# Performance work log

Hardware: AMD Instinct MI355X
Metric: run time of the kernel (lower is better)

Reference implementation:

```python
import jax, jax.numpy as jnp
import numpy as np


def setup_inputs() -> dict:
    key = jax.random.key(0)
    ks = jax.random.split(key, 6)
    B, H, W, C = 2, 96, 96, 64
    x = jax.random.normal(ks[0], (B, H, W, C), dtype=jnp.float32)
    # 1x1 conv weights as [C_in, C_out] matrices (kernel size 1)
    W1 = jax.random.normal(ks[1], (C, C // 8), dtype=jnp.float32) * 0.1
    b1 = jnp.zeros((C // 8,), dtype=jnp.float32)
    W2 = jax.random.normal(ks[2], (C, C // 8), dtype=jnp.float32) * 0.1
    b2 = jnp.zeros((C // 8,), dtype=jnp.float32)
    W3 = jax.random.normal(ks[3], (C, C // 2), dtype=jnp.float32) * 0.1
    b3 = jnp.zeros((C // 2,), dtype=jnp.float32)
    W4 = jax.random.normal(ks[4], (C // 2, C), dtype=jnp.float32) * 0.1
    b4 = jnp.zeros((C,), dtype=jnp.float32)
    gamma = jax.random.uniform(ks[5], (1,), dtype=jnp.float32)
    return {"x": x, "W1": W1, "b1": b1, "W2": W2, "b2": b2,
            "W3": W3, "b3": b3, "W4": W4, "b4": b4, "gamma": gamma}


def reference(x, W1, b1, W2, b2, W3, b3, W4, b4, gamma):
    B, H, W_, C = x.shape
    N = H * W_
    # 1x1 convs == per-pixel matmuls
    f = jnp.einsum('bhwc,cd->bhwd', x, W1) + b1   # [B,H,W,C/8] (key)
    g = jnp.einsum('bhwc,cd->bhwd', x, W2) + b2   # [B,H,W,C/8] (query)
    h = jnp.einsum('bhwc,cd->bhwd', x, W3) + b3   # [B,H,W,C/2] (value)
    f = f.reshape(B, N, -1)
    g = g.reshape(B, N, -1)
    h = h.reshape(B, N, -1)
    s = jnp.einsum('bnd,bmd->bnm', g, f)          # [B,N,N] full score matrix
    beta = jax.nn.softmax(s, axis=-1)
    o = jnp.einsum('bnm,bmd->bnd', beta, h)       # [B,N,C/2]
    o = o.reshape(B, H, W_, C // 2)
    o = jnp.einsum('bhwc,cd->bhwd', o, W4) + b4   # [B,H,W,C]
    return gamma[0] * o + x
```

## Files before the change

### kernel.cpp

```cpp
#include <hip/hip_runtime.h>
#include <hip/hip_bf16.h>


#define BATCH 2
#define NTOK 9216
#define CCH 64
#define DV 32
#define KS 8
#define KEYS_PER_BLOCK (NTOK / KS)
#define KEYS_PER_WAVE (KEYS_PER_BLOCK / 2)
#define KT 32
#define NKT (KEYS_PER_WAVE / KT)
#define ROWS (BATCH * NTOK)
#define QTB (ROWS / 64)
#define NKTILE (NTOK / 32)
#define LOG2E 1.44269504088896340736f
#define PB 32
#define ZTOT 152064

typedef __attribute__((ext_vector_type(8))) short bf16x8;
typedef __attribute__((ext_vector_type(4))) float f32x4;

__device__ __forceinline__ short f2bf(float x) {
    __hip_bfloat16 h = __float2bfloat16(x);
    return *(short*)&h;
}
__device__ __forceinline__ float bf2f(short s) {
    unsigned u = ((unsigned)(unsigned short)s) << 16;
    return *(float*)&u;
}

__global__ __launch_bounds__(512) void proj_kernel(
    const float* __restrict__ x,
    const float* __restrict__ W1, const float* __restrict__ b1,
    const float* __restrict__ W2, const float* __restrict__ b2,
    const float* __restrict__ W3, const float* __restrict__ b3,
    short* __restrict__ fx, short* __restrict__ gx, short* __restrict__ hTi,
    float4* __restrict__ zbase)
{
    __shared__ float xS[PB][CCH];
    __shared__ short fgS[2][PB][32];
    __shared__ short hS[32][PB + 2];

    const int tid = threadIdx.x;
    const int r0  = blockIdx.x * PB;

    {
        int zi = blockIdx.x * 512 + tid;
        if (zi < ZTOT) zbase[zi] = make_float4(0.f, 0.f, 0.f, 0.f);
    }

    ((float4*)xS)[tid] = ((const float4*)(x + (size_t)r0 * CCH))[tid];
    __syncthreads();

    {
        const int half = tid >> 8;
        const int rr   = (tid & 255) >> 3;
        const int c    = tid & 7;
        const float* xr = xS[rr];
        if (half == 0) {
            float acc = b1[c];
            #pragma unroll
            for (int k = 0; k < CCH; ++k) acc += xr[k] * W1[k * 8 + c];
            short hi = f2bf(acc);
            short lo = f2bf(acc - bf2f(hi));
            fgS[0][rr][c] = hi; fgS[0][rr][c + 8] = hi;
            fgS[0][rr][c + 16] = lo; fgS[0][rr][c + 24] = 0;
        } else {
            float acc = b2[c];
            #pragma unroll
            for (int k = 0; k < CCH; ++k) acc += xr[k] * W2[k * 8 + c];
            acc *= LOG2E;
            short hi = f2bf(acc);
            short lo = f2bf(acc - bf2f(hi));
            fgS[1][rr][c] = hi; fgS[1][rr][c + 8] = lo;
            fgS[1][rr][c + 16] = hi; fgS[1][rr][c + 24] = 0;
        }
    }
    {
        const int c = tid & 31;
        const int rbase = tid >> 5;
        #pragma unroll
        for (int s = 0; s < 2; ++s) {
            int rr = rbase + s * 16;
            float acc = b3[c];
            #pragma unroll
            for (int k = 0; k < CCH; ++k) acc += xS[rr][k] * W3[k * 32 + c];
            int np = ((rr & 15) >> 2) * 8 + (rr & 3) + ((rr >> 4) & 1) * 4;
            hS[c][np] = f2bf(acc);
        }
    }
    __syncthreads();

    ((int*)(fx + (size_t)r0 * 32))[tid] = ((const int*)fgS[0])[tid];
    ((int*)(gx + (size_t)r0 * 32))[tid] = ((const int*)fgS[1])[tid];
    {
        const int b  = r0 / NTOK;
        const int n0 = r0 - b * NTOK;
        const int kt = n0 >> 5;
        const int c  = tid >> 4;
        const int d  = tid & 15;
        ((int*)(hTi + ((size_t)(b * NKTILE + kt)) * 1024))[c * 16 + d] =
            ((const int*)&hS[c][0])[d];
    }
}

__global__ __launch_bounds__(128, 4) void attn_kernel(
    const short* __restrict__ fx, const short* __restrict__ gx,
    const short* __restrict__ hTi,
    float* __restrict__ l_acc, float* __restrict__ o_acc)
{
    __shared__ float red[64 * 33];

    const int tid  = threadIdx.x;
    const int wave = tid >> 6;
    const int lane = tid & 63;
    const int col  = lane & 15;
    const int quad = lane >> 4;

    const int blk = blockIdx.x;
    const int qt  = blk % QTB;
    const int ks  = blk / QTB;
    const int b   = qt / (QTB / BATCH);
    const int qbase   = (qt % (QTB / BATCH)) * 64;
    const int rowbase = b * NTOK + qbase;

    const bf16x8 agA = *(const bf16x8*)(gx + (size_t)(rowbase + col) * 32 + quad * 8);
    const bf16x8 agB = *(const bf16x8*)(gx + (size_t)(rowbase + 16 + col) * 32 + quad * 8);
    const bf16x8 agC = *(const bf16x8*)(gx + (size_t)(rowbase + 32 + col) * 32 + quad * 8);
    const bf16x8 agD = *(const bf16x8*)(gx + (size_t)(rowbase + 48 + col) * 32 + quad * 8);

    f32x4 oA0 = {0,0,0,0}, oA1 = {0,0,0,0};
    f32x4 oB0 = {0,0,0,0}, oB1 = {0,0,0,0};
    f32x4 oC0 = {0,0,0,0}, oC1 = {0,0,0,0};
    f32x4 oD0 = {0,0,0,0}, oD1 = {0,0,0,0};
    float lA = 0.f, lB = 0.f, lC = 0.f, lD = 0.f;
    const f32x4 zero4 = {0,0,0,0};

    const int kstart = ks * KEYS_PER_BLOCK + wave * KEYS_PER_WAVE;
    const short* fbase = fx + ((size_t)b * NTOK + kstart) * 32;
    const short* hbase = hTi + ((size_t)(b * NKTILE) + (kstart >> 5)) * 1024
                             + col * 32 + quad * 8;

    bf16x8 fa0 = *(const bf16x8*)(fbase + (size_t)col * 32 + quad * 8);
    bf16x8 fa1 = *(const bf16x8*)(fbase + (size_t)(16 + col) * 32 + quad * 8);
    bf16x8 hb0 = *(const bf16x8*)(hbase);
    bf16x8 hb1 = *(const bf16x8*)(hbase + 512);

    union PU { int i[4]; bf16x8 v; };

    #define EXPPACK(T0, T1, LSUM, P)                                            \
    {                                                                           \
        float e0 = __builtin_amdgcn_exp2f(T0[0]), e1 = __builtin_amdgcn_exp2f(T0[1]); \
        float e2 = __builtin_amdgcn_exp2f(T0[2]), e3 = __builtin_amdgcn_exp2f(T0[3]); \
        float e4 = __builtin_amdgcn_exp2f(T1[0]), e5 = __builtin_amdgcn_exp2f(T1[1]); \
        float e6 = __builtin_amdgcn_exp2f(T1[2]), e7 = __builtin_amdgcn_exp2f(T1[3]); \
        LSUM += (e0 + e1) + (e2 + e3) + (e4 + e5) + (e6 + e7);                  \
        P.i[0] = (int)__builtin_amdgcn_perm((unsigned)__float_as_int(e1) + 0x8000u, \
                                            (unsigned)__float_as_int(e0) + 0x8000u, 0x07060302u); \
        P.i[1] = (int)__builtin_amdgcn_perm((unsigned)__float_as_int(e3) + 0x8000u, \
                                            (unsigned)__float_as_int(e2) + 0x8000u, 0x07060302u); \
        P.i[2] = (int)__builtin_amdgcn_perm((unsigned)__float_as_int(e5) + 0x8000u, \
                                            (unsigned)__float_as_int(e4) + 0x8000u, 0x07060302u); \
        P.i[3] = (int)__builtin_amdgcn_perm((unsigned)__float_as_int(e7) + 0x8000u, \
                                            (unsigned)__float_as_int(e6) + 0x8000u, 0x07060302u); \
    }

    for (int t = 0; t < NKT; ++t) {
        f32x4 tA0 = __builtin_amdgcn_mfma_f32_16x16x32_bf16(fa0, agA, zero4, 0, 0, 0);
        f32x4 tA1 = __builtin_amdgcn_mfma_f32_16x16x32_bf16(fa1, agA, zero4, 0, 0, 0);
        f32x4 tB0 = __builtin_amdgcn_mfma_f32_16x16x32_bf16(fa0, agB, zero4, 0, 0, 0);
        f32x4 tB1 = __builtin_amdgcn_mfma_f32_16x16x32_bf16(fa1, agB, zero4, 0, 0, 0);
        f32x4 tC0 = __builtin_amdgcn_mfma_f32_16x16x32_bf16(fa0, agC, zero4, 0, 0, 0);
        f32x4 tC1 = __builtin_amdgcn_mfma_f32_16x16x32_bf16(fa1, agC, zero4, 0, 0, 0);
        f32x4 tD0 = __builtin_amdgcn_mfma_f32_16x16x32_bf16(fa0, agD, zero4, 0, 0, 0);
        f32x4 tD1 = __builtin_amdgcn_mfma_f32_16x16x32_bf16(fa1, agD, zero4, 0, 0, 0);

        const int kn = (t + 1 < NKT) ? (t + 1) : 0;
        bf16x8 nf0 = *(const bf16x8*)(fbase + (size_t)(kn * KT + col) * 32 + quad * 8);
        bf16x8 nf1 = *(const bf16x8*)(fbase + (size_t)(kn * KT + 16 + col) * 32 + quad * 8);
        bf16x8 nh0 = *(const bf16x8*)(hbase + kn * 1024);
        bf16x8 nh1 = *(const bf16x8*)(hbase + kn * 1024 + 512);

        PU pA, pB, pC, pD;
        EXPPACK(tA0, tA1, lA, pA)
        EXPPACK(tB0, tB1, lB, pB)
        oA0 = __builtin_amdgcn_mfma_f32_16x16x32_bf16(pA.v, hb0, oA0, 0, 0, 0);
        oA1 = __builtin_amdgcn_mfma_f32_16x16x32_bf16(pA.v, hb1, oA1, 0, 0, 0);
        oB0 = __builtin_amdgcn_mfma_f32_16x16x32_bf16(pB.v, hb0, oB0, 0, 0, 0);
        oB1 = __builtin_amdgcn_mfma_f32_16x16x32_bf16(pB.v, hb1, oB1, 0, 0, 0);
        EXPPACK(tC0, tC1, lC, pC)
        EXPPACK(tD0, tD1, lD, pD)
        oC0 = __builtin_amdgcn_mfma_f32_16x16x32_bf16(pC.v, hb0, oC0, 0, 0, 0);
        oC1 = __builtin_amdgcn_mfma_f32_16x16x32_bf16(pC.v, hb1, oC1, 0, 0, 0);
        oD0 = __builtin_amdgcn_mfma_f32_16x16x32_bf16(pD.v, hb0, oD0, 0, 0, 0);
        oD1 = __builtin_amdgcn_mfma_f32_16x16x32_bf16(pD.v, hb1, oD1, 0, 0, 0);

        fa0 = nf0; fa1 = nf1; hb0 = nh0; hb1 = nh1;
    }
    #undef EXPPACK

    lA += __shfl_xor(lA, 16); lA += __shfl_xor(lA, 32);
    lB += __shfl_xor(lB, 16); lB += __shfl_xor(lB, 32);
    lC += __shfl_xor(lC, 16); lC += __shfl_xor(lC, 32);
    lD += __shfl_xor(lD, 16); lD += __shfl_xor(lD, 32);

    if (wave == 1) {
        #pragma unroll
        for (int r = 0; r < 4; ++r) {
            int q = quad * 4 + r;
            red[(q)      * 33 + col]      = oA0[r];
            red[(q)      * 33 + 16 + col] = oA1[r];
            red[(q + 16) * 33 + col]      = oB0[r];
            red[(q + 16) * 33 + 16 + col] = oB1[r];
            red[(q + 32) * 33 + col]      = oC0[r];
            red[(q + 32) * 33 + 16 + col] = oC1[r];
            red[(q + 48) * 33 + col]      = oD0[r];
            red[(q + 48) * 33 + 16 + col] = oD1[r];
        }
        if (quad == 0) {
            red[(col)      * 33 + 32] = lA;
            red[(col + 16) * 33 + 32] = lB;
            red[(col + 32) * 33 + 32] = lC;
            red[(col + 48) * 33 + 32] = lD;
        }
    }
    __syncthreads();
    if (wave == 0) {
        #pragma unroll
        for (int r = 0; r < 4; ++r) {
            int q = quad * 4 + r;
            atomicAdd(&o_acc[(size_t)(rowbase + q)      * 32 + col],      oA0[r] + red[(q)      * 33 + col]);
            atomicAdd(&o_acc[(size_t)(rowbase + q)      * 32 + 16 + col], oA1[r] + red[(q)      * 33 + 16 + col]);
            atomicAdd(&o_acc[(size_t)(rowbase + q + 16) * 32 + col],      oB0[r] + red[(q + 16) * 33 + col]);
            atomicAdd(&o_acc[(size_t)(rowbase + q + 16) * 32 + 16 + col], oB1[r] + red[(q + 16) * 33 + 16 + col]);
            atomicAdd(&o_acc[(size_t)(rowbase + q + 32) * 32 + col],      oC0[r] + red[(q + 32) * 33 + col]);
            atomicAdd(&o_acc[(size_t)(rowbase + q + 32) * 32 + 16 + col], oC1[r] + red[(q + 32) * 33 + 16 + col]);
            atomicAdd(&o_acc[(size_t)(rowbase + q + 48) * 32 + col],      oD0[r] + red[(q + 48) * 33 + col]);
            atomicAdd(&o_acc[(size_t)(rowbase + q + 48) * 32 + 16 + col], oD1[r] + red[(q + 48) * 33 + 16 + col]);
        }
        if (quad == 0) {
            atomicAdd(&l_acc[rowbase + col],      lA + red[(col)      * 33 + 32]);
            atomicAdd(&l_acc[rowbase + 16 + col], lB + red[(col + 16) * 33 + 32]);
            atomicAdd(&l_acc[rowbase + 32 + col], lC + red[(col + 32) * 33 + 32]);
            atomicAdd(&l_acc[rowbase + 48 + col], lD + red[(col + 48) * 33 + 32]);
        }
    }
}

__global__ __launch_bounds__(256) void merge_kernel(
    const float* __restrict__ l_acc, const float* __restrict__ o_acc,
    const float* __restrict__ x,
    const float* __restrict__ W4, const float* __restrict__ b4,
    const float* __restrict__ gamma, float* __restrict__ out)
{
    __shared__ float oS[4][DV];
    int wave = threadIdx.x >> 6;
    int lane = threadIdx.x & 63;
    int row  = blockIdx.x * 4 + wave;

    float invL = 1.f / l_acc[row];
    if (lane < DV) {
        oS[wave][lane] = o_acc[(size_t)row * DV + lane] * invL;
    }
    __syncthreads();

    float dot = b4[lane];
    #pragma unroll
    for (int k = 0; k < DV; ++k) dot += oS[wave][k] * W4[k * 64 + lane];
    float gm  = gamma[0];
    float res = x[(size_t)row * 64 + lane];
    out[(size_t)row * 64 + lane] = gm * dot + res;
}

extern "C" void kernel_launch(void* const* d_in, const int* in_sizes, int n_in,
                              void* d_out, int out_size, void* d_ws, size_t ws_size,
                              hipStream_t stream) {
    const float* x     = (const float*)d_in[0];
    const float* W1    = (const float*)d_in[1];
    const float* b1    = (const float*)d_in[2];
    const float* W2    = (const float*)d_in[3];
    const float* b2    = (const float*)d_in[4];
    const float* W3    = (const float*)d_in[5];
    const float* b3    = (const float*)d_in[6];
    const float* W4    = (const float*)d_in[7];
    const float* b4    = (const float*)d_in[8];
    const float* gamma = (const float*)d_in[9];
    float* out = (float*)d_out;

    short* fx    = (short*)d_ws;
    short* gx    = fx + (size_t)ROWS * 32;
    short* hTi   = gx + (size_t)ROWS * 32;
    float* l_acc = (float*)(hTi + (size_t)ROWS * 32);
    float* o_acc = l_acc + ROWS;

    proj_kernel<<<ROWS / PB, 512, 0, stream>>>(
        x, W1, b1, W2, b2, W3, b3, fx, gx, hTi, (float4*)l_acc);

    attn_kernel<<<QTB * KS, 128, 0, stream>>>(fx, gx, hTi, l_acc, o_acc);

    merge_kernel<<<ROWS / 4, 256, 0, stream>>>(l_acc, o_acc, x, W4, b4, gamma, out);
}
```

Baseline: 139.2 us.

## Split attention keys across four waves, compute row sums via MFMA, pad projection LDS

The attention block grows from two to four waves, each handling a quarter of the block's keys. Partial outputs are combined in shared memory through a sequential three-step reduction with barriers. The softmax denominator moves from per-lane VALU adds to an extra MFMA against a vector of ones, taking work off the vector ALU that also does the exp2. The projection kernel pads its x tile in LDS to reduce bank conflicts. The risks are the added MFMA per tile, extra barriers and reduction rounds, and bf16-rounded row sums.

New measurement: 127.8 us. -8.2%, faster.

```diff
diff --git a/kernel.cpp b/kernel.cpp
--- a/kernel.cpp
+++ b/kernel.cpp
@@ -8,7 +8,7 @@
 #define DV 32
 #define KS 8
 #define KEYS_PER_BLOCK (NTOK / KS)
-#define KEYS_PER_WAVE (KEYS_PER_BLOCK / 2)
+#define KEYS_PER_WAVE (KEYS_PER_BLOCK / 4)
 #define KT 32
 #define NKT (KEYS_PER_WAVE / KT)
 #define ROWS (BATCH * NTOK)
@@ -16,6 +16,7 @@
 #define NKTILE (NTOK / 32)
 #define LOG2E 1.44269504088896340736f
 #define PB 32
+#define XPAD 68
 #define ZTOT 152064
 
 typedef __attribute__((ext_vector_type(8))) short bf16x8;
@@ -38,7 +39,7 @@
     short* __restrict__ fx, short* __restrict__ gx, short* __restrict__ hTi,
     float4* __restrict__ zbase)
 {
-    __shared__ float xS[PB][CCH];
+    __shared__ float xS[PB * XPAD];
     __shared__ short fgS[2][PB][32];
     __shared__ short hS[32][PB + 2];
 
@@ -50,14 +51,18 @@
         if (zi < ZTOT) zbase[zi] = make_float4(0.f, 0.f, 0.f, 0.f);
     }
 
-    ((float4*)xS)[tid] = ((const float4*)(x + (size_t)r0 * CCH))[tid];
+    {
+        const int row = tid >> 4, c4 = tid & 15;
+        ((float4*)(xS + row * XPAD))[c4] =
+            ((const float4*)(x + (size_t)(r0 + row) * CCH))[c4];
+    }
     __syncthreads();
 
     {
         const int half = tid >> 8;
         const int rr   = (tid & 255) >> 3;
         const int c    = tid & 7;
-        const float* xr = xS[rr];
+        const float* xr = xS + rr * XPAD;
         if (half == 0) {
             float acc = b1[c];
             #pragma unroll
@@ -85,7 +90,7 @@
             int rr = rbase + s * 16;
             float acc = b3[c];
             #pragma unroll
-            for (int k = 0; k < CCH; ++k) acc += xS[rr][k] * W3[k * 32 + c];
+            for (int k = 0; k < CCH; ++k) acc += xS[rr * XPAD + k] * W3[k * 32 + c];
             int np = ((rr & 15) >> 2) * 8 + (rr & 3) + ((rr >> 4) & 1) * 4;
             hS[c][np] = f2bf(acc);
         }
@@ -105,7 +110,7 @@
     }
 }
 
-__global__ __launch_bounds__(128, 4) void attn_kernel(
+__global__ __launch_bounds__(256, 4) void attn_kernel(
     const short* __restrict__ fx, const short* __restrict__ gx,
     const short* __restrict__ hTi,
     float* __restrict__ l_acc, float* __restrict__ o_acc)
@@ -130,11 +135,16 @@
     const bf16x8 agC = *(const bf16x8*)(gx + (size_t)(rowbase + 32 + col) * 32 + quad * 8);
     const bf16x8 agD = *(const bf16x8*)(gx + (size_t)(rowbase + 48 + col) * 32 + quad * 8);
 
+    bf16x8 ones;
+    #pragma unroll
+    for (int j = 0; j < 8; ++j) ones[j] = (short)0x3F80;
+
     f32x4 oA0 = {0,0,0,0}, oA1 = {0,0,0,0};
     f32x4 oB0 = {0,0,0,0}, oB1 = {0,0,0,0};
     f32x4 oC0 = {0,0,0,0}, oC1 = {0,0,0,0};
     f32x4 oD0 = {0,0,0,0}, oD1 = {0,0,0,0};
-    float lA = 0.f, lB = 0.f, lC = 0.f, lD = 0.f;
+    f32x4 lfA = {0,0,0,0}, lfB = {0,0,0,0};
+    f32x4 lfC = {0,0,0,0}, lfD = {0,0,0,0};
     const f32x4 zero4 = {0,0,0,0};
 
     const int kstart = ks * KEYS_PER_BLOCK + wave * KEYS_PER_WAVE;
@@ -149,13 +159,12 @@
 
     union PU { int i[4]; bf16x8 v; };
 
-    #define EXPPACK(T0, T1, LSUM, P)                                            \
+    #define EXPPACK(T0, T1, P)                                                  \
     {                                                                           \
         float e0 = __builtin_amdgcn_exp2f(T0[0]), e1 = __builtin_amdgcn_exp2f(T0[1]); \
         float e2 = __builtin_amdgcn_exp2f(T0[2]), e3 = __builtin_amdgcn_exp2f(T0[3]); \
         float e4 = __builtin_amdgcn_exp2f(T1[0]), e5 = __builtin_amdgcn_exp2f(T1[1]); \
         float e6 = __builtin_amdgcn_exp2f(T1[2]), e7 = __builtin_amdgcn_exp2f(T1[3]); \
-        LSUM += (e0 + e1) + (e2 + e3) + (e4 + e5) + (e6 + e7);                  \
         P.i[0] = (int)__builtin_amdgcn_perm((unsigned)__float_as_int(e1) + 0x8000u, \
                                             (unsigned)__float_as_int(e0) + 0x8000u, 0x07060302u); \
         P.i[1] = (int)__builtin_amdgcn_perm((unsigned)__float_as_int(e3) + 0x8000u, \
@@ -183,67 +192,95 @@
         bf16x8 nh1 = *(const bf16x8*)(hbase + kn * 1024 + 512);
 
         PU pA, pB, pC, pD;
-        EXPPACK(tA0, tA1, lA, pA)
-        EXPPACK(tB0, tB1, lB, pB)
+        EXPPACK(tA0, tA1, pA)
+        EXPPACK(tB0, tB1, pB)
         oA0 = __builtin_amdgcn_mfma_f32_16x16x32_bf16(pA.v, hb0, oA0, 0, 0, 0);
         oA1 = __builtin_amdgcn_mfma_f32_16x16x32_bf16(pA.v, hb1, oA1, 0, 0, 0);
+        lfA = __builtin_amdgcn_mfma_f32_16x16x32_bf16(pA.v, ones, lfA, 0, 0, 0);
         oB0 = __builtin_amdgcn_mfma_f32_16x16x32_bf16(pB.v, hb0, oB0, 0, 0, 0);
         oB1 = __builtin_amdgcn_mfma_f32_16x16x32_bf16(pB.v, hb1, oB1, 0, 0, 0);
-        EXPPACK(tC0, tC1, lC, pC)
-        EXPPACK(tD0, tD1, lD, pD)
+        lfB = __builtin_amdgcn_mfma_f32_16x16x32_bf16(pB.v, ones, lfB, 0, 0, 0);
+        EXPPACK(tC0, tC1, pC)
+        EXPPACK(tD0, tD1, pD)
         oC0 = __builtin_amdgcn_mfma_f32_16x16x32_bf16(pC.v, hb0, oC0, 0, 0, 0);
         oC1 = __builtin_amdgcn_mfma_f32_16x16x32_bf16(pC.v, hb1, oC1, 0, 0, 0);
+        lfC = __builtin_amdgcn_mfma_f32_16x16x32_bf16(pC.v, ones, lfC, 0, 0, 0);
         oD0 = __builtin_amdgcn_mfma_f32_16x16x32_bf16(pD.v, hb0, oD0, 0, 0, 0);
         oD1 = __builtin_amdgcn_mfma_f32_16x16x32_bf16(pD.v, hb1, oD1, 0, 0, 0);
+        lfD = __builtin_amdgcn_mfma_f32_16x16x32_bf16(pD.v, ones, lfD, 0, 0, 0);
 
         fa0 = nf0; fa1 = nf1; hb0 = nh0; hb1 = nh1;
     }
     #undef EXPPACK
 
-    lA += __shfl_xor(lA, 16); lA += __shfl_xor(lA, 32);
-    lB += __shfl_xor(lB, 16); lB += __shfl_xor(lB, 32);
-    lC += __shfl_xor(lC, 16); lC += __shfl_xor(lC, 32);
-    lD += __shfl_xor(lD, 16); lD += __shfl_xor(lD, 32);
-
-    if (wave == 1) {
-        #pragma unroll
-        for (int r = 0; r < 4; ++r) {
-            int q = quad * 4 + r;
-            red[(q)      * 33 + col]      = oA0[r];
-            red[(q)      * 33 + 16 + col] = oA1[r];
-            red[(q + 16) * 33 + col]      = oB0[r];
-            red[(q + 16) * 33 + 16 + col] = oB1[r];
-            red[(q + 32) * 33 + col]      = oC0[r];
-            red[(q + 32) * 33 + 16 + col] = oC1[r];
-            red[(q + 48) * 33 + col]      = oD0[r];
-            red[(q + 48) * 33 + 16 + col] = oD1[r];
-        }
-        if (quad == 0) {
-            red[(col)      * 33 + 32] = lA;
-            red[(col + 16) * 33 + 32] = lB;
-            red[(col + 32) * 33 + 32] = lC;
-            red[(col + 48) * 33 + 32] = lD;
-        }
-    }
-    __syncthreads();
+    for (int w = 1; w < 4; ++w) {
+        if (wave == w) {
+            #pragma unroll
+            for (int r = 0; r < 4; ++r) {
+                int q = quad * 4 + r;
+                red[(q)      * 33 + col]      = oA0[r];
+                red[(q)      * 33 + 16 + col] = oA1[r];
+                red[(q + 16) * 33 + col]      = oB0[r];
+                red[(q + 16) * 33 + 16 + col] = oB1[r];
+                red[(q + 32) * 33 + col]      = oC0[r];
+                red[(q + 32) * 33 + 16 + col] = oC1[r];
+                red[(q + 48) * 33 + col]      = oD0[r];
+                red[(q + 48) * 33 + 16 + col] = oD1[r];
+            }
+            if (col == 0) {
+                #pragma unroll
+                for (int r = 0; r < 4; ++r) {
+                    int q = quad * 4 + r;
+                    red[(q)      * 33 + 32] = lfA[r];
+                    red[(q + 16) * 33 + 32] = lfB[r];
+                    red[(q + 32) * 33 + 32] = lfC[r];
+                    red[(q + 48) * 33 + 32] = lfD[r];
+                }
+            }
+        }
+        __syncthreads();
+        if (wave == 0) {
+            #pragma unroll
+            for (int r = 0; r < 4; ++r) {
+                int q = quad * 4 + r;
+                oA0[r] += red[(q)      * 33 + col];
+                oA1[r] += red[(q)      * 33 + 16 + col];
+                oB0[r] += red[(q + 16) * 33 + col];
+                oB1[r] += red[(q + 16) * 33 + 16 + col];
+                oC0[r] += red[(q + 32) * 33 + col];
+                oC1[r] += red[(q + 32) * 33 + 16 + col];
+                oD0[r] += red[(q + 48) * 33 + col];
+                oD1[r] += red[(q + 48) * 33 + 16 + col];
+                lfA[r] += red[(q)      * 33 + 32];
+                lfB[r] += red[(q + 16) * 33 + 32];
+                lfC[r] += red[(q + 32) * 33 + 32];
+                lfD[r] += red[(q + 48) * 33 + 32];
+            }
+        }
+        __syncthreads();
+    }
     if (wave == 0) {
         #pragma unroll
         for (int r = 0; r < 4; ++r) {
             int q = quad * 4 + r;
-            atomicAdd(&o_acc[(size_t)(rowbase + q)      * 32 + col],      oA0[r] + red[(q)      * 33 + col]);
-            atomicAdd(&o_acc[(size_t)(rowbase + q)      * 32 + 16 + col], oA1[r] + red[(q)      * 33 + 16 + col]);
-            atomicAdd(&o_acc[(size_t)(rowbase + q + 16) * 32 + col],      oB0[r] + red[(q + 16) * 33 + col]);
-            atomicAdd(&o_acc[(size_t)(rowbase + q + 16) * 32 + 16 + col], oB1[r] + red[(q + 16) * 33 + 16 + col]);
-            atomicAdd(&o_acc[(size_t)(rowbase + q + 32) * 32 + col],      oC0[r] + red[(q + 32) * 33 + col]);
-            atomicAdd(&o_acc[(size_t)(rowbase + q + 32) * 32 + 16 + col], oC1[r] + red[(q + 32) * 33 + 16 + col]);
-            atomicAdd(&o_acc[(size_t)(rowbase + q + 48) * 32 + col],      oD0[r] + red[(q + 48) * 33 + col]);
-            atomicAdd(&o_acc[(size_t)(rowbase + q + 48) * 32 + 16 + col], oD1[r] + red[(q + 48) * 33 + 16 + col]);
-        }
-        if (quad == 0) {
-            atomicAdd(&l_acc[rowbase + col],      lA + red[(col)      * 33 + 32]);
-            atomicAdd(&l_acc[rowbase + 16 + col], lB + red[(col + 16) * 33 + 32]);
-            atomicAdd(&l_acc[rowbase + 32 + col], lC + red[(col + 32) * 33 + 32]);
-            atomicAdd(&l_acc[rowbase + 48 + col], lD + red[(col + 48) * 33 + 32]);
+            atomicAdd(&o_acc[(size_t)(rowbase + q)      * 32 + col],      oA0[r]);
+            atomicAdd(&o_acc[(size_t)(rowbase + q)      * 32 + 16 + col], oA1[r]);
+            atomicAdd(&o_acc[(size_t)(rowbase + q + 16) * 32 + col],      oB0[r]);
+            atomicAdd(&o_acc[(size_t)(rowbase + q + 16) * 32 + 16 + col], oB1[r]);
+            atomicAdd(&o_acc[(size_t)(rowbase + q + 32) * 32 + col],      oC0[r]);
+            atomicAdd(&o_acc[(size_t)(rowbase + q + 32) * 32 + 16 + col], oC1[r]);
+            atomicAdd(&o_acc[(size_t)(rowbase + q + 48) * 32 + col],      oD0[r]);
+            atomicAdd(&o_acc[(size_t)(rowbase + q + 48) * 32 + 16 + col], oD1[r]);
+        }
+        if (col == 0) {
+            #pragma unroll
+            for (int r = 0; r < 4; ++r) {
+                int q = quad * 4 + r;
+                atomicAdd(&l_acc[rowbase + q],      lfA[r]);
+                atomicAdd(&l_acc[rowbase + q + 16], lfB[r]);
+                atomicAdd(&l_acc[rowbase + q + 32], lfC[r]);
+                atomicAdd(&l_acc[rowbase + q + 48], lfD[r]);
+            }
         }
     }
 }
@@ -297,7 +334,7 @@
     proj_kernel<<<ROWS / PB, 512, 0, stream>>>(
         x, W1, b1, W2, b2, W3, b3, fx, gx, hTi, (float4*)l_acc);
 
-    attn_kernel<<<QTB * KS, 128, 0, stream>>>(fx, gx, hTi, l_acc, o_acc);
+    attn_kernel<<<QTB * KS, 256, 0, stream>>>(fx, gx, hTi, l_acc, o_acc);
 
     merge_kernel<<<ROWS / 4, 256, 0, stream>>>(l_acc, o_acc, x, W4, b4, gamma, out);
 }
```
